# Performance work log

Hardware: AMD Instinct MI355X
Metric: run time of the kernel (lower is better)

The kernel has to match this reference:

```python
import jax, jax.numpy as jnp
import numpy as np

HEAD = 8  # number of attention heads (init kwarg)


def setup_inputs() -> dict:
    key = jax.random.key(0)
    k1, k2, k3 = jax.random.split(key, 3)
    b, H, W, c = 8, 32, 32, 512
    dim = 512
    x = jax.random.normal(k1, (b, H, W, c), dtype=jnp.float32)
    # 1x1 Conv == per-pixel matmul over channels
    w_qkv = jax.random.normal(k2, (c, 3 * dim), dtype=jnp.float32) * (c ** -0.5)
    w_out = jax.random.normal(k3, (dim, dim), dtype=jnp.float32) * (dim ** -0.5)
    b_out = jnp.zeros((dim,), dtype=jnp.float32)
    return {"x": x, "w_qkv": w_qkv, "w_out": w_out, "b_out": b_out}


def reference(x, w_qkv, w_out, b_out):
    b, H, W, c = x.shape
    n = H * W
    # QKV 1x1-conv projection (no bias)
    qkv = jnp.einsum('bhwc,cd->bhwd', x, w_qkv)          # (b, H, W, 3*dim)
    qkv = qkv.reshape(b, n, HEAD, -1)                     # (b, n, head, 3*dh)
    q, k, v = jnp.split(qkv, 3, axis=-1)                  # each (b, n, head, dh)
    scale = b ** -0.5  # NOTE: source scales by batch size, reproduced faithfully
    attn = jax.nn.softmax(jnp.einsum('bihd,bjhd->bhij', q, k) * scale, axis=-1)
    out = jnp.einsum('bhij,bjhd->bihd', attn, v)          # (b, n, head, dh)
    out = out.reshape(b, H, W, -1)                        # (b, H, W, dim)
    # output 1x1-conv projection (with bias)
    return jnp.einsum('bhwc,cd->bhwd', out, w_out) + b_out
```

## Files before the change

kernel.cpp:

```cpp
#include <hip/hip_runtime.h>
#include <hip/hip_bf16.h>

typedef __bf16 bf16x8_t __attribute__((ext_vector_type(8)));
typedef float  f32x4_t  __attribute__((ext_vector_type(4)));
typedef short  s16x8_t  __attribute__((ext_vector_type(8)));

#define NTOK   1024
#define CDIM   512
#define QKVDIM 1536
#define NHEAD  8
#define DHEAD  64
#define SCALE  0.35355339059327373f
#define FIXM   24.0f

__device__ __forceinline__ float b2f(short s) {
    unsigned int u = ((unsigned int)(unsigned short)s) << 16;
    float f; __builtin_memcpy(&f, &u, 4); return f;
}
__device__ __forceinline__ short f2b(float f) {
    __bf16 h = (__bf16)f; short s; __builtin_memcpy(&s, &h, 2); return s;
}

__global__ __launch_bounds__(256) void cvt(const float* __restrict__ in,
                                           short* __restrict__ out, int n8)
{
    int i = blockIdx.x * 256 + threadIdx.x;
    if (i < n8) {
        const float* p = in + (size_t)i * 8;
        float4 a = *(const float4*)p, b = *(const float4*)(p + 4);
        s16x8_t v;
        v[0]=f2b(a.x); v[1]=f2b(a.y); v[2]=f2b(a.z); v[3]=f2b(a.w);
        v[4]=f2b(b.x); v[5]=f2b(b.y); v[6]=f2b(b.z); v[7]=f2b(b.w);
        *(s16x8_t*)(out + (size_t)i * 8) = v;
    }
}

__global__ __launch_bounds__(256) void cvtT(const float* __restrict__ in,
                                            short* __restrict__ out,
                                            int K, int N)
{
    int i = blockIdx.x * 256 + threadIdx.x;
    if (i < K * N) {
        int k = i / N, n = i % N;
        out[(size_t)n * K + k] = f2b(in[i]);
    }
}

template <int N, bool BIAS, bool OUTF32>
__global__ __launch_bounds__(256) void gemm128(
    const short* __restrict__ A, const short* __restrict__ Bt,
    const float* __restrict__ bias, void* __restrict__ C)
{
    __shared__ __align__(16) short Al[128 * 64];
    __shared__ __align__(16) short Bl[128 * 64];

    const int t = threadIdx.x;
    const int N0 = blockIdx.x * 128, M0 = blockIdx.y * 128;
    const int w = t >> 6, lane = t & 63;
    const int quad = lane >> 4, mr = lane & 15;
    const int wm = (w >> 1) * 64, wn = (w & 1) * 64;

    int srow[4], soff[4];
#pragma unroll
    for (int r = 0; r < 4; ++r) {
        int ci = r * 256 + t;
        srow[r] = ci >> 3;
        soff[r] = (ci & 7) * 8;
    }
    const short* Ag = A  + (size_t)M0 * 512;
    const short* Bg = Bt + (size_t)N0 * 512;

    s16x8_t ar[4], br[4];
#pragma unroll
    for (int r = 0; r < 4; ++r) {
        ar[r] = *(const s16x8_t*)(Ag + (size_t)srow[r] * 512 + soff[r]);
        br[r] = *(const s16x8_t*)(Bg + (size_t)srow[r] * 512 + soff[r]);
    }

    f32x4_t acc[4][4];
#pragma unroll
    for (int ms = 0; ms < 4; ++ms)
#pragma unroll
        for (int ns = 0; ns < 4; ++ns) acc[ms][ns] = f32x4_t{0.f,0.f,0.f,0.f};

#pragma unroll 1
    for (int kc = 0; kc < 8; ++kc) {
        __syncthreads();
#pragma unroll
        for (int r = 0; r < 4; ++r) {
            int lds = srow[r] * 64 + (((soff[r] >> 3) ^ (srow[r] & 7)) * 8);
            *(s16x8_t*)(Al + lds) = ar[r];
            *(s16x8_t*)(Bl + lds) = br[r];
        }
        __syncthreads();
        if (kc < 7) {
            int k0 = (kc + 1) * 64;
#pragma unroll
            for (int r = 0; r < 4; ++r) {
                ar[r] = *(const s16x8_t*)(Ag + (size_t)srow[r] * 512 + k0 + soff[r]);
                br[r] = *(const s16x8_t*)(Bg + (size_t)srow[r] * 512 + k0 + soff[r]);
            }
        }
#pragma unroll
        for (int kh = 0; kh < 2; ++kh) {
            bf16x8_t af[4], bf[4];
#pragma unroll
            for (int ms = 0; ms < 4; ++ms) {
                int rr = wm + ms * 16 + mr;
                af[ms] = *(const bf16x8_t*)(Al + rr * 64 + (((kh * 4 + quad) ^ (rr & 7)) * 8));
            }
#pragma unroll
            for (int ns = 0; ns < 4; ++ns) {
                int rr = wn + ns * 16 + mr;
                bf[ns] = *(const bf16x8_t*)(Bl + rr * 64 + (((kh * 4 + quad) ^ (rr & 7)) * 8));
            }
#pragma unroll
            for (int ms = 0; ms < 4; ++ms)
#pragma unroll
                for (int ns = 0; ns < 4; ++ns)
                    acc[ms][ns] = __builtin_amdgcn_mfma_f32_16x16x32_bf16(
                        af[ms], bf[ns], acc[ms][ns], 0, 0, 0);
        }
    }

#pragma unroll
    for (int ms = 0; ms < 4; ++ms) {
        int row = M0 + wm + ms * 16 + quad * 4;
#pragma unroll
        for (int ns = 0; ns < 4; ++ns) {
            int col = N0 + wn + ns * 16 + mr;
            float bz = BIAS ? bias[col] : 0.f;
#pragma unroll
            for (int i = 0; i < 4; ++i) {
                if constexpr (OUTF32)
                    ((float*)C)[(size_t)(row + i) * N + col] = acc[ms][ns][i] + bz;
                else
                    ((short*)C)[(size_t)(row + i) * N + col] = f2b(acc[ms][ns][i]);
            }
        }
    }
}

__global__ __launch_bounds__(256) void attn_mfma(
    const short* __restrict__ qkv, short* __restrict__ aout)
{
    __shared__ __align__(16) short Kl[64 * 72];
    __shared__ __align__(16) short Vt[64 * 72];
    __shared__ __align__(16) short Pl[4][16 * 72];

    const int t = threadIdx.x;
    const int qt = blockIdx.x, h = blockIdx.y, b = blockIdx.z;
    const int w = t >> 6, lane = t & 63;
    const int quad = lane >> 4, mr = lane & 15;

    const size_t qrow = (size_t)(b * NTOK + qt * 64 + w * 16 + mr) * QKVDIM + h * 192;
    const bf16x8_t qf0 = *(const bf16x8_t*)(qkv + qrow + quad * 8);
    const bf16x8_t qf1 = *(const bf16x8_t*)(qkv + qrow + 32 + quad * 8);

    float lsum[4] = {0.f, 0.f, 0.f, 0.f};
    f32x4_t O[4];
#pragma unroll
    for (int d = 0; d < 4; ++d) O[d] = f32x4_t{0.f, 0.f, 0.f, 0.f};

    short* Pw = Pl[w];

    const int j0i = t >> 3, j1i = j0i + 32, d8 = (t & 7) * 8;
    const int pjb0 = ((j0i >> 3) ^ (t & 7)) * 8 + (j0i & 7);
    const int pjb1 = ((j1i >> 3) ^ (t & 7)) * 8 + (j1i & 7);

    s16x8_t k0r, v0r, k1r, v1r;
    {
        size_t b0 = (size_t)(b * NTOK + j0i) * QKVDIM + h * 192;
        size_t b1 = (size_t)(b * NTOK + j1i) * QKVDIM + h * 192;
        k0r = *(const s16x8_t*)(qkv + b0 + 64 + d8);
        v0r = *(const s16x8_t*)(qkv + b0 + 128 + d8);
        k1r = *(const s16x8_t*)(qkv + b1 + 64 + d8);
        v1r = *(const s16x8_t*)(qkv + b1 + 128 + d8);
    }

#pragma unroll 1
    for (int jt = 0; jt < 16; ++jt) {
        __syncthreads();
        *(s16x8_t*)(Kl + j0i * 72 + d8) = k0r;
        *(s16x8_t*)(Kl + j1i * 72 + d8) = k1r;
#pragma unroll
        for (int i = 0; i < 8; ++i) {
            Vt[(d8 + i) * 72 + pjb0] = v0r[i];
            Vt[(d8 + i) * 72 + pjb1] = v1r[i];
        }
        __syncthreads();

        if (jt < 15) {
            size_t b0 = (size_t)(b * NTOK + (jt + 1) * 64 + j0i) * QKVDIM + h * 192;
            size_t b1 = (size_t)(b * NTOK + (jt + 1) * 64 + j1i) * QKVDIM + h * 192;
            k0r = *(const s16x8_t*)(qkv + b0 + 64 + d8);
            v0r = *(const s16x8_t*)(qkv + b0 + 128 + d8);
            k1r = *(const s16x8_t*)(qkv + b1 + 64 + d8);
            v1r = *(const s16x8_t*)(qkv + b1 + 128 + d8);
        }

        f32x4_t s[4];
#pragma unroll
        for (int js = 0; js < 4; ++js) {
            const short* kb = Kl + (js * 16 + mr) * 72 + quad * 8;
            f32x4_t a0 = __builtin_amdgcn_mfma_f32_16x16x32_bf16(
                qf0, *(const bf16x8_t*)kb, f32x4_t{0.f,0.f,0.f,0.f}, 0, 0, 0);
            s[js] = __builtin_amdgcn_mfma_f32_16x16x32_bf16(
                qf1, *(const bf16x8_t*)(kb + 32), a0, 0, 0, 0);
        }

        float pr[4][4];
#pragma unroll
        for (int js = 0; js < 4; ++js)
#pragma unroll
            for (int r = 0; r < 4; ++r) {
                float p = b2f(f2b(__expf(s[js][r] * SCALE - FIXM)));
                pr[js][r] = p;
                lsum[r] += p;
            }

#pragma unroll
        for (int js = 0; js < 4; ++js)
#pragma unroll
            for (int r = 0; r < 4; ++r)
                Pw[(quad * 4 + r) * 72 + js * 16 + mr] = f2b(pr[js][r]);
        bf16x8_t pa0 = *(const bf16x8_t*)(Pw + mr * 72 + quad * 8);
        bf16x8_t pa1 = *(const bf16x8_t*)(Pw + mr * 72 + 32 + quad * 8);

#pragma unroll
        for (int d = 0; d < 4; ++d) {
            int R = d * 16 + mr;
            int rx = (R >> 3) & 7;
            const short* vb0 = Vt + R * 72 + ((quad ^ rx) * 8);
            const short* vb1 = Vt + R * 72 + (((4 + quad) ^ rx) * 8);
            O[d] = __builtin_amdgcn_mfma_f32_16x16x32_bf16(
                pa0, *(const bf16x8_t*)vb0, O[d], 0, 0, 0);
            O[d] = __builtin_amdgcn_mfma_f32_16x16x32_bf16(
                pa1, *(const bf16x8_t*)vb1, O[d], 0, 0, 0);
        }
    }

#pragma unroll
    for (int r = 0; r < 4; ++r) {
        float l = lsum[r];
#pragma unroll
        for (int off = 1; off < 16; off <<= 1) l += __shfl_xor(l, off);
        float inv = 1.f / l;
        size_t tok = (size_t)(b * NTOK + qt * 64 + w * 16 + quad * 4 + r);
#pragma unroll
        for (int d = 0; d < 4; ++d)
            aout[tok * CDIM + h * DHEAD + d * 16 + mr] = f2b(O[d][r] * inv);
    }
}

extern "C" void kernel_launch(void* const* d_in, const int* in_sizes, int n_in,
                              void* d_out, int out_size, void* d_ws, size_t ws_size,
                              hipStream_t stream)
{
    const float* x     = (const float*)d_in[0];
    const float* w_qkv = (const float*)d_in[1];
    const float* w_out = (const float*)d_in[2];
    const float* b_out = (const float*)d_in[3];
    for (int i = 0; i < n_in; ++i) {
        if      (in_sizes[i] == 4194304) x     = (const float*)d_in[i];
        else if (in_sizes[i] ==  786432) w_qkv = (const float*)d_in[i];
        else if (in_sizes[i] ==  262144) w_out = (const float*)d_in[i];
        else if (in_sizes[i] ==     512) b_out = (const float*)d_in[i];
    }

    short* qkv  = (short*)d_ws;
    short* aout = (short*)((char*)d_ws + (size_t)8192 * QKVDIM * 2);
    short* xb   = (short*)d_out;
    short* wqbT = (short*)d_out + (size_t)8192 * 512;
    short* wobT = (short*)d_ws;

    cvt <<<2048, 256, 0, stream>>>(x, xb, 4194304 / 8);
    cvtT<<<3072, 256, 0, stream>>>(w_qkv, wqbT, 512, QKVDIM);

    gemm128<QKVDIM, false, false>
        <<<dim3(QKVDIM / 128, 8192 / 128), 256, 0, stream>>>(xb, wqbT, nullptr, qkv);

    attn_mfma<<<dim3(16, NHEAD, 8), 256, 0, stream>>>(qkv, aout);

    cvtT<<<1024, 256, 0, stream>>>(w_out, wobT, 512, 512);

    gemm128<CDIM, true, true>
        <<<dim3(CDIM / 128, 8192 / 128), 256, 0, stream>>>(aout, wobT, b_out, d_out);
}
```

Baseline: 155.5 us.

## Fuse x fp32-to-bf16 conversion into QKV GEMM, remap attention grid, swizzle P

```diff
diff --git a/kernel.cpp b/kernel.cpp
--- a/kernel.cpp
+++ b/kernel.cpp
@@ -10,8 +10,8 @@
 #define QKVDIM 1536
 #define NHEAD  8
 #define DHEAD  64
-#define SCALE  0.35355339059327373f
-#define FIXM   24.0f
+#define C1EXP  0.51007088f
+#define C2EXP  34.624681f
 
 __device__ __forceinline__ float b2f(short s) {
     unsigned int u = ((unsigned int)(unsigned short)s) << 16;
@@ -19,20 +19,6 @@
 }
 __device__ __forceinline__ short f2b(float f) {
     __bf16 h = (__bf16)f; short s; __builtin_memcpy(&s, &h, 2); return s;
-}
-
-__global__ __launch_bounds__(256) void cvt(const float* __restrict__ in,
-                                           short* __restrict__ out, int n8)
-{
-    int i = blockIdx.x * 256 + threadIdx.x;
-    if (i < n8) {
-        const float* p = in + (size_t)i * 8;
-        float4 a = *(const float4*)p, b = *(const float4*)(p + 4);
-        s16x8_t v;
-        v[0]=f2b(a.x); v[1]=f2b(a.y); v[2]=f2b(a.z); v[3]=f2b(a.w);
-        v[4]=f2b(b.x); v[5]=f2b(b.y); v[6]=f2b(b.z); v[7]=f2b(b.w);
-        *(s16x8_t*)(out + (size_t)i * 8) = v;
-    }
 }
 
 __global__ __launch_bounds__(256) void cvtT(const float* __restrict__ in,
@@ -46,9 +32,9 @@
     }
 }
 
-template <int N, bool BIAS, bool OUTF32>
+template <int N, bool BIAS, bool AF32, bool OUTF32>
 __global__ __launch_bounds__(256) void gemm128(
-    const short* __restrict__ A, const short* __restrict__ Bt,
+    const void* __restrict__ A, const short* __restrict__ Bt,
     const float* __restrict__ bias, void* __restrict__ C)
 {
     __shared__ __align__(16) short Al[128 * 64];
@@ -67,13 +53,18 @@
         srow[r] = ci >> 3;
         soff[r] = (ci & 7) * 8;
     }
-    const short* Ag = A  + (size_t)M0 * 512;
     const short* Bg = Bt + (size_t)N0 * 512;
 
     s16x8_t ar[4], br[4];
+    float4 arf[4][2];
 #pragma unroll
     for (int r = 0; r < 4; ++r) {
-        ar[r] = *(const s16x8_t*)(Ag + (size_t)srow[r] * 512 + soff[r]);
+        if constexpr (AF32) {
+            const float* p = (const float*)A + (size_t)(M0 + srow[r]) * 512 + soff[r];
+            arf[r][0] = *(const float4*)p; arf[r][1] = *(const float4*)(p + 4);
+        } else {
+            ar[r] = *(const s16x8_t*)((const short*)A + (size_t)(M0 + srow[r]) * 512 + soff[r]);
+        }
         br[r] = *(const s16x8_t*)(Bg + (size_t)srow[r] * 512 + soff[r]);
     }
 
@@ -89,7 +80,16 @@
 #pragma unroll
         for (int r = 0; r < 4; ++r) {
             int lds = srow[r] * 64 + (((soff[r] >> 3) ^ (srow[r] & 7)) * 8);
-            *(s16x8_t*)(Al + lds) = ar[r];
+            if constexpr (AF32) {
+                s16x8_t v;
+                v[0]=f2b(arf[r][0].x); v[1]=f2b(arf[r][0].y);
+                v[2]=f2b(arf[r][0].z); v[3]=f2b(arf[r][0].w);
+                v[4]=f2b(arf[r][1].x); v[5]=f2b(arf[r][1].y);
+                v[6]=f2b(arf[r][1].z); v[7]=f2b(arf[r][1].w);
+                *(s16x8_t*)(Al + lds) = v;
+            } else {
+                *(s16x8_t*)(Al + lds) = ar[r];
+            }
             *(s16x8_t*)(Bl + lds) = br[r];
         }
         __syncthreads();
@@ -97,7 +97,12 @@
             int k0 = (kc + 1) * 64;
 #pragma unroll
             for (int r = 0; r < 4; ++r) {
-                ar[r] = *(const s16x8_t*)(Ag + (size_t)srow[r] * 512 + k0 + soff[r]);
+                if constexpr (AF32) {
+                    const float* p = (const float*)A + (size_t)(M0 + srow[r]) * 512 + k0 + soff[r];
+                    arf[r][0] = *(const float4*)p; arf[r][1] = *(const float4*)(p + 4);
+                } else {
+                    ar[r] = *(const s16x8_t*)((const short*)A + (size_t)(M0 + srow[r]) * 512 + k0 + soff[r]);
+                }
                 br[r] = *(const s16x8_t*)(Bg + (size_t)srow[r] * 512 + k0 + soff[r]);
             }
         }
@@ -149,7 +154,10 @@
     __shared__ __align__(16) short Pl[4][16 * 72];
 
     const int t = threadIdx.x;
-    const int qt = blockIdx.x, h = blockIdx.y, b = blockIdx.z;
+    const int g = blockIdx.x;
+    const int qt = (g >> 3) & 15;
+    const int bh = ((g >> 7) << 3) | (g & 7);
+    const int h = bh & 7, b = bh >> 3;
     const int w = t >> 6, lane = t & 63;
     const int quad = lane >> 4, mr = lane & 15;
 
@@ -209,23 +217,24 @@
                 qf1, *(const bf16x8_t*)(kb + 32), a0, 0, 0, 0);
         }
 
-        float pr[4][4];
+        short ph[4][4];
 #pragma unroll
         for (int js = 0; js < 4; ++js)
 #pragma unroll
             for (int r = 0; r < 4; ++r) {
-                float p = b2f(f2b(__expf(s[js][r] * SCALE - FIXM)));
-                pr[js][r] = p;
-                lsum[r] += p;
+                short hh = f2b(__builtin_amdgcn_exp2f(s[js][r] * C1EXP - C2EXP));
+                ph[js][r] = hh;
+                lsum[r] += b2f(hh);
             }
 
 #pragma unroll
         for (int js = 0; js < 4; ++js)
 #pragma unroll
             for (int r = 0; r < 4; ++r)
-                Pw[(quad * 4 + r) * 72 + js * 16 + mr] = f2b(pr[js][r]);
-        bf16x8_t pa0 = *(const bf16x8_t*)(Pw + mr * 72 + quad * 8);
-        bf16x8_t pa1 = *(const bf16x8_t*)(Pw + mr * 72 + 32 + quad * 8);
+                Pw[(quad * 4 + r) * 72 +
+                   (((js * 2 + (mr >> 3)) + 2 * quad) & 7) * 8 + (mr & 7)] = ph[js][r];
+        bf16x8_t pa0 = *(const bf16x8_t*)(Pw + mr * 72 + ((quad     + 2 * (mr >> 2)) & 7) * 8);
+        bf16x8_t pa1 = *(const bf16x8_t*)(Pw + mr * 72 + ((quad + 4 + 2 * (mr >> 2)) & 7) * 8);
 
 #pragma unroll
         for (int d = 0; d < 4; ++d) {
@@ -270,20 +279,18 @@
 
     short* qkv  = (short*)d_ws;
     short* aout = (short*)((char*)d_ws + (size_t)8192 * QKVDIM * 2);
-    short* xb   = (short*)d_out;
-    short* wqbT = (short*)d_out + (size_t)8192 * 512;
+    short* wqbT = (short*)d_out;
     short* wobT = (short*)d_ws;
 
-    cvt <<<2048, 256, 0, stream>>>(x, xb, 4194304 / 8);
     cvtT<<<3072, 256, 0, stream>>>(w_qkv, wqbT, 512, QKVDIM);
 
-    gemm128<QKVDIM, false, false>
-        <<<dim3(QKVDIM / 128, 8192 / 128), 256, 0, stream>>>(xb, wqbT, nullptr, qkv);
-
-    attn_mfma<<<dim3(16, NHEAD, 8), 256, 0, stream>>>(qkv, aout);
+    gemm128<QKVDIM, false, true, false>
+        <<<dim3(QKVDIM / 128, 8192 / 128), 256, 0, stream>>>(x, wqbT, nullptr, qkv);
+
+    attn_mfma<<<1024, 256, 0, stream>>>(qkv, aout);
 
     cvtT<<<1024, 256, 0, stream>>>(w_out, wobT, 512, 512);
 
-    gemm128<CDIM, true, true>
+    gemm128<CDIM, true, false, true>
         <<<dim3(CDIM / 128, 8192 / 128), 256, 0, stream>>>(aout, wobT, b_out, d_out);
 }
```

Measured after the change: 158.0 us. No clear change (+1.6%).

## Fuse input conversions, double-buffer K/V, and process 128 queries per attention block

Applied to the files above, without the earlier changes.

```diff
diff --git a/kernel.cpp b/kernel.cpp
--- a/kernel.cpp
+++ b/kernel.cpp
@@ -10,8 +10,8 @@
 #define QKVDIM 1536
 #define NHEAD  8
 #define DHEAD  64
-#define SCALE  0.35355339059327373f
-#define FIXM   24.0f
+#define C1EXP  0.51007088f
+#define C2EXP  34.624681f
 
 __device__ __forceinline__ float b2f(short s) {
     unsigned int u = ((unsigned int)(unsigned short)s) << 16;
@@ -21,17 +21,23 @@
     __bf16 h = (__bf16)f; short s; __builtin_memcpy(&s, &h, 2); return s;
 }
 
-__global__ __launch_bounds__(256) void cvt(const float* __restrict__ in,
-                                           short* __restrict__ out, int n8)
-{
-    int i = blockIdx.x * 256 + threadIdx.x;
-    if (i < n8) {
-        const float* p = in + (size_t)i * 8;
+__global__ __launch_bounds__(256) void cvt_fused(
+    const float* __restrict__ x, const float* __restrict__ wq,
+    short* __restrict__ xb, short* __restrict__ wqbT)
+{
+    int bid = blockIdx.x;
+    if (bid < 2048) {
+        int i = bid * 256 + threadIdx.x;
+        const float* p = x + (size_t)i * 8;
         float4 a = *(const float4*)p, b = *(const float4*)(p + 4);
         s16x8_t v;
         v[0]=f2b(a.x); v[1]=f2b(a.y); v[2]=f2b(a.z); v[3]=f2b(a.w);
         v[4]=f2b(b.x); v[5]=f2b(b.y); v[6]=f2b(b.z); v[7]=f2b(b.w);
-        *(s16x8_t*)(out + (size_t)i * 8) = v;
+        *(s16x8_t*)(xb + (size_t)i * 8) = v;
+    } else {
+        int i = (bid - 2048) * 256 + threadIdx.x;
+        int k = i / QKVDIM, n = i % QKVDIM;
+        wqbT[(size_t)n * 512 + k] = f2b(wq[i]);
     }
 }
 
@@ -144,23 +150,32 @@
 __global__ __launch_bounds__(256) void attn_mfma(
     const short* __restrict__ qkv, short* __restrict__ aout)
 {
-    __shared__ __align__(16) short Kl[64 * 72];
-    __shared__ __align__(16) short Vt[64 * 72];
-    __shared__ __align__(16) short Pl[4][16 * 72];
+    __shared__ __align__(16) short Kb[2][64 * 72];
+    __shared__ __align__(16) short Vb[2][64 * 72];
+    __shared__ __align__(16) short Pl[4][32 * 72];
 
     const int t = threadIdx.x;
-    const int qt = blockIdx.x, h = blockIdx.y, b = blockIdx.z;
+    const int g = blockIdx.x;
+    const int qb = (g >> 3) & 7;
+    const int bh = ((g >> 6) << 3) | (g & 7);
+    const int h = bh & 7, b = bh >> 3;
     const int w = t >> 6, lane = t & 63;
     const int quad = lane >> 4, mr = lane & 15;
 
-    const size_t qrow = (size_t)(b * NTOK + qt * 64 + w * 16 + mr) * QKVDIM + h * 192;
-    const bf16x8_t qf0 = *(const bf16x8_t*)(qkv + qrow + quad * 8);
-    const bf16x8_t qf1 = *(const bf16x8_t*)(qkv + qrow + 32 + quad * 8);
-
-    float lsum[4] = {0.f, 0.f, 0.f, 0.f};
-    f32x4_t O[4];
-#pragma unroll
-    for (int d = 0; d < 4; ++d) O[d] = f32x4_t{0.f, 0.f, 0.f, 0.f};
+    bf16x8_t qf[2][2];
+#pragma unroll
+    for (int ms = 0; ms < 2; ++ms) {
+        size_t qrow = (size_t)(b * NTOK + qb * 128 + w * 32 + ms * 16 + mr) * QKVDIM + h * 192;
+        qf[ms][0] = *(const bf16x8_t*)(qkv + qrow + quad * 8);
+        qf[ms][1] = *(const bf16x8_t*)(qkv + qrow + 32 + quad * 8);
+    }
+
+    float lsum[2][4] = {};
+    f32x4_t O[2][4];
+#pragma unroll
+    for (int ms = 0; ms < 2; ++ms)
+#pragma unroll
+        for (int d = 0; d < 4; ++d) O[ms][d] = f32x4_t{0.f, 0.f, 0.f, 0.f};
 
     short* Pw = Pl[w];
 
@@ -180,7 +195,9 @@
 
 #pragma unroll 1
     for (int jt = 0; jt < 16; ++jt) {
-        __syncthreads();
+        const int cur = jt & 1;
+        short* Kl = Kb[cur];
+        short* Vt = Vb[cur];
         *(s16x8_t*)(Kl + j0i * 72 + d8) = k0r;
         *(s16x8_t*)(Kl + j1i * 72 + d8) = k1r;
 #pragma unroll
@@ -199,58 +216,65 @@
             v1r = *(const s16x8_t*)(qkv + b1 + 128 + d8);
         }
 
-        f32x4_t s[4];
-#pragma unroll
-        for (int js = 0; js < 4; ++js) {
-            const short* kb = Kl + (js * 16 + mr) * 72 + quad * 8;
-            f32x4_t a0 = __builtin_amdgcn_mfma_f32_16x16x32_bf16(
-                qf0, *(const bf16x8_t*)kb, f32x4_t{0.f,0.f,0.f,0.f}, 0, 0, 0);
-            s[js] = __builtin_amdgcn_mfma_f32_16x16x32_bf16(
-                qf1, *(const bf16x8_t*)(kb + 32), a0, 0, 0, 0);
-        }
-
-        float pr[4][4];
-#pragma unroll
-        for (int js = 0; js < 4; ++js)
-#pragma unroll
-            for (int r = 0; r < 4; ++r) {
-                float p = b2f(f2b(__expf(s[js][r] * SCALE - FIXM)));
-                pr[js][r] = p;
-                lsum[r] += p;
-            }
-
-#pragma unroll
-        for (int js = 0; js < 4; ++js)
-#pragma unroll
-            for (int r = 0; r < 4; ++r)
-                Pw[(quad * 4 + r) * 72 + js * 16 + mr] = f2b(pr[js][r]);
-        bf16x8_t pa0 = *(const bf16x8_t*)(Pw + mr * 72 + quad * 8);
-        bf16x8_t pa1 = *(const bf16x8_t*)(Pw + mr * 72 + 32 + quad * 8);
-
-#pragma unroll
-        for (int d = 0; d < 4; ++d) {
-            int R = d * 16 + mr;
-            int rx = (R >> 3) & 7;
-            const short* vb0 = Vt + R * 72 + ((quad ^ rx) * 8);
-            const short* vb1 = Vt + R * 72 + (((4 + quad) ^ rx) * 8);
-            O[d] = __builtin_amdgcn_mfma_f32_16x16x32_bf16(
-                pa0, *(const bf16x8_t*)vb0, O[d], 0, 0, 0);
-            O[d] = __builtin_amdgcn_mfma_f32_16x16x32_bf16(
-                pa1, *(const bf16x8_t*)vb1, O[d], 0, 0, 0);
-        }
-    }
-
-#pragma unroll
-    for (int r = 0; r < 4; ++r) {
-        float l = lsum[r];
-#pragma unroll
-        for (int off = 1; off < 16; off <<= 1) l += __shfl_xor(l, off);
-        float inv = 1.f / l;
-        size_t tok = (size_t)(b * NTOK + qt * 64 + w * 16 + quad * 4 + r);
-#pragma unroll
-        for (int d = 0; d < 4; ++d)
-            aout[tok * CDIM + h * DHEAD + d * 16 + mr] = f2b(O[d][r] * inv);
-    }
+#pragma unroll
+        for (int ms = 0; ms < 2; ++ms) {
+            f32x4_t s[4];
+#pragma unroll
+            for (int js = 0; js < 4; ++js) {
+                const short* kb = Kl + (js * 16 + mr) * 72 + quad * 8;
+                f32x4_t a0 = __builtin_amdgcn_mfma_f32_16x16x32_bf16(
+                    qf[ms][0], *(const bf16x8_t*)kb, f32x4_t{0.f,0.f,0.f,0.f}, 0, 0, 0);
+                s[js] = __builtin_amdgcn_mfma_f32_16x16x32_bf16(
+                    qf[ms][1], *(const bf16x8_t*)(kb + 32), a0, 0, 0, 0);
+            }
+
+            short ph[4][4];
+#pragma unroll
+            for (int js = 0; js < 4; ++js)
+#pragma unroll
+                for (int r = 0; r < 4; ++r) {
+                    short hh = f2b(__builtin_amdgcn_exp2f(s[js][r] * C1EXP - C2EXP));
+                    ph[js][r] = hh;
+                    lsum[ms][r] += b2f(hh);
+                }
+
+            short* Pm = Pw + ms * 16 * 72;
+#pragma unroll
+            for (int js = 0; js < 4; ++js)
+#pragma unroll
+                for (int r = 0; r < 4; ++r)
+                    Pm[(quad * 4 + r) * 72 +
+                       (((js * 2 + (mr >> 3)) + 2 * quad) & 7) * 8 + (mr & 7)] = ph[js][r];
+            bf16x8_t pa0 = *(const bf16x8_t*)(Pm + mr * 72 + ((quad     + 2 * (mr >> 2)) & 7) * 8);
+            bf16x8_t pa1 = *(const bf16x8_t*)(Pm + mr * 72 + ((quad + 4 + 2 * (mr >> 2)) & 7) * 8);
+
+#pragma unroll
+            for (int d = 0; d < 4; ++d) {
+                int R = d * 16 + mr;
+                int rx = (R >> 3) & 7;
+                const short* vb0 = Vt + R * 72 + ((quad ^ rx) * 8);
+                const short* vb1 = Vt + R * 72 + (((4 + quad) ^ rx) * 8);
+                O[ms][d] = __builtin_amdgcn_mfma_f32_16x16x32_bf16(
+                    pa0, *(const bf16x8_t*)vb0, O[ms][d], 0, 0, 0);
+                O[ms][d] = __builtin_amdgcn_mfma_f32_16x16x32_bf16(
+                    pa1, *(const bf16x8_t*)vb1, O[ms][d], 0, 0, 0);
+            }
+        }
+    }
+
+#pragma unroll
+    for (int ms = 0; ms < 2; ++ms)
+#pragma unroll
+        for (int r = 0; r < 4; ++r) {
+            float l = lsum[ms][r];
+#pragma unroll
+            for (int off = 1; off < 16; off <<= 1) l += __shfl_xor(l, off);
+            float inv = 1.f / l;
+            size_t tok = (size_t)(b * NTOK + qb * 128 + w * 32 + ms * 16 + quad * 4 + r);
+#pragma unroll
+            for (int d = 0; d < 4; ++d)
+                aout[tok * CDIM + h * DHEAD + d * 16 + mr] = f2b(O[ms][d][r] * inv);
+        }
 }
 
 extern "C" void kernel_launch(void* const* d_in, const int* in_sizes, int n_in,
@@ -274,13 +298,12 @@
     short* wqbT = (short*)d_out + (size_t)8192 * 512;
     short* wobT = (short*)d_ws;
 
-    cvt <<<2048, 256, 0, stream>>>(x, xb, 4194304 / 8);
-    cvtT<<<3072, 256, 0, stream>>>(w_qkv, wqbT, 512, QKVDIM);
+    cvt_fused<<<5120, 256, 0, stream>>>(x, w_qkv, xb, wqbT);
 
     gemm128<QKVDIM, false, false>
         <<<dim3(QKVDIM / 128, 8192 / 128), 256, 0, stream>>>(xb, wqbT, nullptr, qkv);
 
-    attn_mfma<<<dim3(16, NHEAD, 8), 256, 0, stream>>>(qkv, aout);
+    attn_mfma<<<512, 256, 0, stream>>>(qkv, aout);
 
     cvtT<<<1024, 256, 0, stream>>>(w_out, wobT, 512, 512);
 
```

After: 152.1 us. -2.1%, faster.
